# Kernel tuning notes

Hardware: AMD Instinct MI355X
Metric: run time of the kernel (lower is better)

The kernel has to match this reference:

```python
import jax, jax.numpy as jnp
import numpy as np
from jax import lax

B, H, W = 4096, 8, 8
DICT, SE, E, NZ = 64, 8, 256, 1024
C1, C2 = 64, 128
EPS = 1e-4


def setup_inputs() -> dict:
    key = jax.random.key(0)
    ks = jax.random.split(key, 32)
    d = {}
    d['s'] = jax.random.randint(ks[0], (B, H, W), 0, DICT)
    d['s_prime'] = jax.random.randint(ks[1], (B, H, W), 0, DICT)
    d['w_embed'] = jax.random.normal(ks[2], (DICT, SE), dtype=jnp.float32)
    i = 3
    for p in ('p1', 'p2', 'p3'):
        d[p + '_w1'] = jax.random.normal(ks[i], (C1, SE, 3, 3), dtype=jnp.float32) * 0.1; i += 1
        d[p + '_b1'] = jax.random.normal(ks[i], (C1,), dtype=jnp.float32) * 0.1; i += 1
        d[p + '_w2'] = jax.random.normal(ks[i], (C2, C1, 3, 3), dtype=jnp.float32) * 0.05; i += 1
        d[p + '_b2'] = jax.random.normal(ks[i], (C2,), dtype=jnp.float32) * 0.05; i += 1
        d[p + '_lw'] = jax.random.normal(ks[i], (E, C2 * H * W), dtype=jnp.float32) * 0.02; i += 1
        d[p + '_lb'] = jax.random.normal(ks[i], (E,), dtype=jnp.float32) * 0.02; i += 1
    d['z_vectors'] = jax.random.normal(ks[i], (NZ, E), dtype=jnp.float32)
    d['scale'] = jnp.ones((1,), dtype=jnp.float32)
    return d


def _conv(x, w, b):
    # x: [B,C,H,W], w: [O,I,3,3], padding=1 == SAME for k=3
    y = lax.conv_general_dilated(x, w, (1, 1), 'SAME',
                                 dimension_numbers=('NCHW', 'OIHW', 'NCHW'))
    return y + b[None, :, None, None]


def _phi(x, w1, b1, w2, b2, lw, lb):
    # run_modules(..., last_activation=True): relu after every conv
    x = jax.nn.relu(_conv(x, w1, b1))
    x = jax.nn.relu(_conv(x, w2, b2))
    x = x.reshape(x.shape[0], -1)  # [B, C2*H*W]
    return x @ lw.T + lb  # [B, E]


def _normalized(m, eps):
    return m / (jnp.sqrt(jnp.sum(m * m, axis=1, keepdims=True)) + eps)


def reference(s, s_prime, w_embed,
              p1_w1, p1_b1, p1_w2, p1_b2, p1_lw, p1_lb,
              p2_w1, p2_b1, p2_w2, p2_b2, p2_lw, p2_lb,
              p3_w1, p3_b1, p3_w2, p3_b2, p3_lw, p3_lb,
              z_vectors, scale):
    # nn.Embedding(max_norm=1): renorm rows with norm > 1 to unit norm
    wn = jnp.sqrt(jnp.sum(w_embed * w_embed, axis=1, keepdims=True))
    w = w_embed * jnp.minimum(1.0, 1.0 / jnp.maximum(wn, 1e-7))
    s_embed = jnp.transpose(w[s], (0, 3, 1, 2))        # [B,SE,H,W]
    sp_embed = jnp.transpose(w[s_prime], (0, 3, 1, 2))  # embed_conv is None -> identity

    s_int = _phi(s_embed, p1_w1, p1_b1, p1_w2, p1_b2, p1_lw, p1_lb)            # phi1
    diff_int = _phi(sp_embed - s_embed, p2_w1, p2_b1, p2_w2, p2_b2, p2_lw, p2_lb)  # phi2
    sp_out = _normalized(_phi(sp_embed, p3_w1, p3_b1, p3_w2, p3_b2, p3_lw, p3_lb), EPS)  # phi3

    # quantize: cdist (p=2) against codebook, argmax (farthest, as in source), gather
    x2 = jnp.sum(diff_int * diff_int, axis=1, keepdims=True)      # [B,1]
    z2 = jnp.sum(z_vectors * z_vectors, axis=1)[None, :]          # [1,NZ]
    dist = jnp.sqrt(jnp.maximum(x2 + z2 - 2.0 * (diff_int @ z_vectors.T), 0.0))  # [B,NZ]
    z_inds = jnp.argmax(dist, axis=1)                              # [B]
    z_matrix = z_vectors[z_inds]                                   # [B,E]

    s_out = _normalized(s_int + z_matrix, EPS)                     # fc (fc_sizes=None)
    gram = s_out @ sp_out.T                                        # [B,B]
    return jnp.exp(scale) * gram
```

## Files before the change

kernel.cpp:

```cpp
#include <hip/hip_runtime.h>
#include <hip/hip_bf16.h>
#include <math.h>

#define NB 4096
#define SE 8
#define ND 64
#define C1 64
#define C2 128
#define NE 256
#define NZ 1024
#define CHUNK 2048
#define KACT 8192
#define KSPLIT 8

#define W1M_N (3*12*64*8)
#define W2M_N (3*18*128*32)
#define ZT_N  (256*1024)
#define PREP_TOTAL (W1M_N + W2M_N + ZT_N)
#define PREP_TOTAL2 (PREP_TOTAL + 512)
#define LW_N (NE*KACT)

typedef __attribute__((ext_vector_type(8))) short bf16x8;
typedef __attribute__((ext_vector_type(4))) float f32x4;
typedef __attribute__((ext_vector_type(8))) unsigned short u16x8;
typedef __attribute__((ext_vector_type(4))) unsigned short u16x4;

static __device__ __forceinline__ unsigned short f2bf(float v) {
  __hip_bfloat16 h = __float2bfloat16(v);
  return __builtin_bit_cast(unsigned short, h);
}
static __device__ __forceinline__ float bf2f(unsigned short u) {
  return __bfloat162float(__builtin_bit_cast(__hip_bfloat16, u));
}

__global__ __launch_bounds__(256) void prep_kernel(
    const float* __restrict__ w1_0, const float* __restrict__ w1_1, const float* __restrict__ w1_2,
    const float* __restrict__ w2_0, const float* __restrict__ w2_1, const float* __restrict__ w2_2,
    const float* __restrict__ z, const float* __restrict__ w_embed,
    unsigned short* __restrict__ w1mh, unsigned short* __restrict__ w1ml,
    unsigned short* __restrict__ w2mh, unsigned short* __restrict__ w2ml,
    float* __restrict__ zT, float* __restrict__ wnorm)
{
  int idx = blockIdx.x * 256 + threadIdx.x;
  if (idx < W1M_N) {
    int p = idx / 6144; int r = idx - p*6144;
    int j = r >> 9; int rem = r & 511; int o = rem >> 3; int c = rem & 7;
    const float* w1 = (p == 0) ? w1_0 : (p == 1) ? w1_1 : w1_2;
    float v = (j < 9) ? w1[o*72 + c*9 + j] : 0.f;
    unsigned short h = f2bf(v);
    w1mh[idx] = h;
    w1ml[idx] = f2bf(v - bf2f(h));
  } else if (idx < W1M_N + W2M_N) {
    int r0 = idx - W1M_N;
    int p = r0 / (128*576); int r = r0 - p*(128*576);
    int o = r / 576; int rem = r - o*576; int j = rem >> 6; int c = rem & 63;
    const float* w2 = (p == 0) ? w2_0 : (p == 1) ? w2_1 : w2_2;
    float v = w2[o*576 + c*9 + j];
    unsigned short h = f2bf(v);
    const int d = p*(128*576) + ((j << 1) + (c >> 5))*4096 + o*32 + (c & 31);
    w2mh[d] = h;
    w2ml[d] = f2bf(v - bf2f(h));
  } else if (idx < PREP_TOTAL) {
    int r = idx - (W1M_N + W2M_N);
    int e = r >> 10, n = r & 1023;
    zT[r] = z[n*256 + e];
  } else if (idx < PREP_TOTAL2) {
    int t = idx - PREP_TOTAL;
    int o = t >> 3, c = t & 7;
    float ss = 0.f;
    #pragma unroll
    for (int e = 0; e < 8; ++e) { float u = w_embed[o*8 + e]; ss += u*u; }
    float nrm = sqrtf(ss);
    float sc = fminf(1.f, 1.f / fmaxf(nrm, 1e-7f));
    wnorm[o*8 + c] = w_embed[o*8 + c] * sc;
  }
}

__global__ __launch_bounds__(256) void prep_lw_kernel(
    const float* __restrict__ lw, unsigned short* __restrict__ lwh,
    unsigned short* __restrict__ lwl, int do_lo)
{
  int idx = blockIdx.x * 256 + threadIdx.x;
  float v = lw[idx];
  unsigned short h = f2bf(v);
  lwh[idx] = h;
  if (do_lo) lwl[idx] = f2bf(v - bf2f(h));
}

template<int PASSES>
__global__ __launch_bounds__(256, 4) void conv_phi_kernel(
    const int* __restrict__ s, const int* __restrict__ sp,
    const float* __restrict__ wnorm,
    const unsigned short* __restrict__ w1mh, const unsigned short* __restrict__ w1ml,
    const float* __restrict__ b1,
    const unsigned short* __restrict__ w2mh, const unsigned short* __restrict__ w2ml,
    const float* __restrict__ b2,
    unsigned short* __restrict__ acth, unsigned short* __restrict__ actl,
    int mode, int b_start)
{
  __shared__ __align__(16) unsigned short xph[960];
  __shared__ __align__(16) unsigned short xpl[960];
  __shared__ __align__(16) unsigned short c1h[7680];
  __shared__ __align__(16) unsigned short c1l[7680];

  const int tid = threadIdx.x;
  const int b = b_start + blockIdx.x;

  {
    int4 z4 = {0,0,0,0};
    for (int t = tid; t < 120; t += 256) { ((int4*)xph)[t] = z4; ((int4*)xpl)[t] = z4; }
    for (int t = tid; t < 960; t += 256) { ((int4*)c1h)[t] = z4; ((int4*)c1l)[t] = z4; }
  }
  __syncthreads();

  if (tid < 64) {
    const int si  = s[b*64 + tid];
    const int spi = sp[b*64 + tid];
    const float4 a0 = *(const float4*)(wnorm + si*8);
    const float4 a1v = *(const float4*)(wnorm + si*8 + 4);
    const float4 c0 = *(const float4*)(wnorm + spi*8);
    const float4 c1v = *(const float4*)(wnorm + spi*8 + 4);
    float e0[8] = {a0.x,a0.y,a0.z,a0.w, a1v.x,a1v.y,a1v.z,a1v.w};
    float e1[8] = {c0.x,c0.y,c0.z,c0.w, c1v.x,c1v.y,c1v.z,c1v.w};
    u16x8 hv, lv;
    #pragma unroll
    for (int c = 0; c < SE; ++c) {
      float v = (mode == 0) ? e0[c] : (mode == 1) ? (e1[c] - e0[c]) : e1[c];
      unsigned short h = f2bf(v);
      hv[c] = h;
      lv[c] = f2bf(v - bf2f(h));
    }
    const int lin = ((tid >> 3) + 1)*12 + (tid & 7) + 1;
    *(u16x8*)(xph + lin*8) = hv;
    *(u16x8*)(xpl + lin*8) = lv;
  }
  __syncthreads();

  {
    const int lane = tid & 63, wid = tid >> 6;
    const int ph = wid;
    const int l15 = lane & 15, lk4 = lane >> 4;

    f32x4 a1[4];
    #pragma unroll
    for (int fm = 0; fm < 4; ++fm) a1[fm] = (f32x4){0.f,0.f,0.f,0.f};

    #pragma unroll
    for (int kk = 0; kk < 3; ++kk) {
      const int j = (kk << 2) + lk4;
      const int jc = (j > 8) ? 8 : j;
      const int dy = jc / 3, dx = jc - 3*(jc/3);
      bf16x8 Wh[4], Wl[4];
      #pragma unroll
      for (int fm = 0; fm < 4; ++fm) {
        const int o = (fm << 4) + l15;
        Wh[fm] = *(const bf16x8*)(w1mh + (j << 9) + (o << 3));
        Wl[fm] = *(const bf16x8*)(w1ml + (j << 9) + (o << 3));
      }
      const int p = (ph << 4) + l15;
      const int lin = ((p >> 3) + dy)*12 + (p & 7) + dx;
      const bf16x8 Xh = *(const bf16x8*)(xph + (lin << 3));
      const bf16x8 Xl = *(const bf16x8*)(xpl + (lin << 3));
      __builtin_amdgcn_s_setprio(1);
      #pragma unroll
      for (int fm = 0; fm < 4; ++fm) {
        a1[fm] = __builtin_amdgcn_mfma_f32_16x16x32_bf16(Wh[fm], Xh, a1[fm], 0, 0, 0);
        a1[fm] = __builtin_amdgcn_mfma_f32_16x16x32_bf16(Wl[fm], Xh, a1[fm], 0, 0, 0);
        a1[fm] = __builtin_amdgcn_mfma_f32_16x16x32_bf16(Wh[fm], Xl, a1[fm], 0, 0, 0);
      }
      __builtin_amdgcn_s_setprio(0);
    }

    const int p = (ph << 4) + l15;
    const int lin = ((p >> 3) + 1)*12 + (p & 7) + 1;
    #pragma unroll
    for (int fm = 0; fm < 4; ++fm) {
      const int obase = (fm << 4) + (lk4 << 2);
      const float4 bv = *(const float4*)(b1 + obase);
      const int idx2 = (obase >> 3)*960 + lin*8 + (obase & 7);
      u16x4 hv, lv;
      {
        float v0 = fmaxf(a1[fm][0] + bv.x, 0.f);
        float v1 = fmaxf(a1[fm][1] + bv.y, 0.f);
        float v2 = fmaxf(a1[fm][2] + bv.z, 0.f);
        float v3 = fmaxf(a1[fm][3] + bv.w, 0.f);
        hv[0] = f2bf(v0); hv[1] = f2bf(v1); hv[2] = f2bf(v2); hv[3] = f2bf(v3);
        lv[0] = f2bf(v0 - bf2f(hv[0])); lv[1] = f2bf(v1 - bf2f(hv[1]));
        lv[2] = f2bf(v2 - bf2f(hv[2])); lv[3] = f2bf(v3 - bf2f(hv[3]));
      }
      *(u16x4*)(c1h + idx2) = hv;
      *(u16x4*)(c1l + idx2) = lv;
    }
  }
  __syncthreads();

  {
    const int lane = tid & 63, wid = tid >> 6;
    const int ob = wid << 5;
    const int l15 = lane & 15, lk4 = lane >> 4;
    const int y0b = l15 >> 3, x0 = l15 & 7;

    f32x4 acc[4][2];
    #pragma unroll
    for (int mf = 0; mf < 4; ++mf)
      #pragma unroll
      for (int nf = 0; nf < 2; ++nf) acc[mf][nf] = (f32x4){0.f,0.f,0.f,0.f};

    #pragma unroll
    for (int j = 0; j < 9; ++j) {
      const int dy = j / 3, dx = j - 3*(j/3);
      #pragma unroll
      for (int h2 = 0; h2 < 2; ++h2) {
        const int sbase = ((j << 1) + h2) << 12;
        bf16x8 Bh[2], Bl[2];
        #pragma unroll
        for (int nf = 0; nf < 2; ++nf) {
          const int orow = ob + (nf << 4) + l15;
          const int a = sbase + orow*32 + (lk4 << 3);
          Bh[nf] = *(const bf16x8*)(w2mh + a);
          if (PASSES == 3) Bl[nf] = *(const bf16x8*)(w2ml + a);
        }
        const int cbk = (h2 << 2) + lk4;
        bf16x8 Ah[4], Al[4];
        #pragma unroll
        for (int mf = 0; mf < 4; ++mf) {
          const int lin = ((mf << 1) + y0b + dy)*12 + x0 + dx;
          const int a = cbk*960 + (lin << 3);
          Ah[mf] = *(const bf16x8*)(c1h + a);
          Al[mf] = *(const bf16x8*)(c1l + a);
        }
        __builtin_amdgcn_s_setprio(1);
        #pragma unroll
        for (int mf = 0; mf < 4; ++mf) {
          #pragma unroll
          for (int nf = 0; nf < 2; ++nf) {
            acc[mf][nf] = __builtin_amdgcn_mfma_f32_16x16x32_bf16(Ah[mf], Bh[nf], acc[mf][nf], 0, 0, 0);
            acc[mf][nf] = __builtin_amdgcn_mfma_f32_16x16x32_bf16(Al[mf], Bh[nf], acc[mf][nf], 0, 0, 0);
            if (PASSES == 3)
              acc[mf][nf] = __builtin_amdgcn_mfma_f32_16x16x32_bf16(Ah[mf], Bl[nf], acc[mf][nf], 0, 0, 0);
          }
        }
        __builtin_amdgcn_s_setprio(0);
      }
    }

    const size_t rowbase = (size_t)blockIdx.x * 8192;
    #pragma unroll
    for (int nf = 0; nf < 2; ++nf) {
      const int col = ob + (nf << 4) + l15;
      const float bv = b2[col];
      #pragma unroll
      for (int mf = 0; mf < 4; ++mf) {
        const int p0 = mf*16 + lk4*4;
        u16x4 hv, lv;
        #pragma unroll
        for (int r2 = 0; r2 < 4; ++r2) {
          float v = fmaxf(acc[mf][nf][r2] + bv, 0.f);
          unsigned short hq = f2bf(v);
          hv[r2] = hq;
          lv[r2] = f2bf(v - bf2f(hq));
        }
        *(u16x4*)(acth + rowbase + col*64 + p0) = hv;
        if (PASSES == 3)
          *(u16x4*)(actl + rowbase + col*64 + p0) = lv;
      }
    }
  }
}

template<int PASSES>
__global__ __launch_bounds__(256) void gemm_lds_tn(
    const unsigned short* __restrict__ Ahp, const unsigned short* __restrict__ Alp,
    const unsigned short* __restrict__ Bhp, const unsigned short* __restrict__ Blp,
    int K, float* __restrict__ Cdirect, float* __restrict__ Cpart,
    const float* __restrict__ bias, const float* __restrict__ scale_ptr)
{
  constexpr int NOP = (PASSES == 3) ? 2 : 1;
  __shared__ __align__(16) unsigned short As[NOP][128*64];
  __shared__ __align__(16) unsigned short Bs[NOP][64*64];

  const int tid = threadIdx.x;
  const int lane = tid & 63, wid = tid >> 6;
  const int wm = wid >> 1, wn = wid & 1;
  const int l15 = lane & 15, lk4 = lane >> 4;
  const int M = gridDim.x << 7, N = gridDim.y << 6;
  const int KC = K / gridDim.z;
  const int bm = blockIdx.x << 7, bn = blockIdx.y << 6;
  const int kbase = blockIdx.z * KC;
  const int NT = KC >> 6;

  const int sr = tid >> 3;
  const int sc8 = (tid & 7) * 8;

  const unsigned short* gA[NOP];
  const unsigned short* gB[NOP];
  gA[0] = Ahp; gB[0] = Bhp;
  if (PASSES == 3) { gA[1] = Alp; gB[1] = Blp; }

  u16x8 ra[NOP][4], rb[NOP][2];

  f32x4 acc[4][2];
  #pragma unroll
  for (int fm = 0; fm < 4; ++fm)
    #pragma unroll
    for (int nf = 0; nf < 2; ++nf) acc[fm][nf] = (f32x4){0.f,0.f,0.f,0.f};

  {
    const int k0 = kbase + sc8;
    #pragma unroll
    for (int p = 0; p < NOP; ++p) {
      #pragma unroll
      for (int i = 0; i < 4; ++i)
        ra[p][i] = *(const u16x8*)(gA[p] + (size_t)(bm + sr + i*32) * K + k0);
      #pragma unroll
      for (int i = 0; i < 2; ++i)
        rb[p][i] = *(const u16x8*)(gB[p] + (size_t)(bn + sr + i*32) * K + k0);
    }
  }

  for (int t = 0; t < NT; ++t) {
    __syncthreads();
    #pragma unroll
    for (int p = 0; p < NOP; ++p) {
      #pragma unroll
      for (int i = 0; i < 4; ++i) {
        const int r = sr + i*32;
        *(u16x8*)(&As[p][r*64 + (sc8 ^ ((r & 7) << 3))]) = ra[p][i];
      }
      #pragma unroll
      for (int i = 0; i < 2; ++i) {
        const int r = sr + i*32;
        *(u16x8*)(&Bs[p][r*64 + (sc8 ^ ((r & 7) << 3))]) = rb[p][i];
      }
    }
    __syncthreads();
    if (t + 1 < NT) {
      const int k0 = kbase + ((t + 1) << 6) + sc8;
      #pragma unroll
      for (int p = 0; p < NOP; ++p) {
        #pragma unroll
        for (int i = 0; i < 4; ++i)
          ra[p][i] = *(const u16x8*)(gA[p] + (size_t)(bm + sr + i*32) * K + k0);
        #pragma unroll
        for (int i = 0; i < 2; ++i)
          rb[p][i] = *(const u16x8*)(gB[p] + (size_t)(bn + sr + i*32) * K + k0);
      }
    }
    #pragma unroll
    for (int ks = 0; ks < 2; ++ks) {
      const int kb = ks*32 + lk4*8;
      bf16x8 af[NOP][4], bf[NOP][2];
      #pragma unroll
      for (int p = 0; p < NOP; ++p) {
        #pragma unroll
        for (int fm = 0; fm < 4; ++fm) {
          const int r = wm*64 + fm*16 + l15;
          af[p][fm] = *(const bf16x8*)(&As[p][r*64 + (kb ^ ((r & 7) << 3))]);
        }
        #pragma unroll
        for (int nf = 0; nf < 2; ++nf) {
          const int r = wn*32 + nf*16 + l15;
          bf[p][nf] = *(const bf16x8*)(&Bs[p][r*64 + (kb ^ ((r & 7) << 3))]);
        }
      }
      #pragma unroll
      for (int fm = 0; fm < 4; ++fm) {
        #pragma unroll
        for (int nf = 0; nf < 2; ++nf) {
          acc[fm][nf] = __builtin_amdgcn_mfma_f32_16x16x32_bf16(af[0][fm], bf[0][nf], acc[fm][nf], 0, 0, 0);
          if (PASSES == 3) {
            acc[fm][nf] = __builtin_amdgcn_mfma_f32_16x16x32_bf16(af[0][fm], bf[1][nf], acc[fm][nf], 0, 0, 0);
            acc[fm][nf] = __builtin_amdgcn_mfma_f32_16x16x32_bf16(af[1][fm], bf[0][nf], acc[fm][nf], 0, 0, 0);
          }
        }
      }
    }
  }

  if (Cpart) {
    float* base = Cpart + (size_t)blockIdx.z * ((size_t)M * N);
    #pragma unroll
    for (int fm = 0; fm < 4; ++fm) {
      #pragma unroll
      for (int nf = 0; nf < 2; ++nf) {
        const int row0 = bm + wm*64 + fm*16 + lk4*4;
        const int col  = bn + wn*32 + nf*16 + l15;
        #pragma unroll
        for (int r2 = 0; r2 < 4; ++r2)
          base[(size_t)(row0 + r2) * N + col] = acc[fm][nf][r2];
      }
    }
  } else {
    float alpha = scale_ptr ? expf(scale_ptr[0]) : 1.f;
    #pragma unroll
    for (int fm = 0; fm < 4; ++fm) {
      #pragma unroll
      for (int nf = 0; nf < 2; ++nf) {
        const int row0 = bm + wm*64 + fm*16 + lk4*4;
        const int col  = bn + wn*32 + nf*16 + l15;
        const float bv = bias ? bias[col] : 0.f;
        #pragma unroll
        for (int r2 = 0; r2 < 4; ++r2)
          Cdirect[(size_t)(row0 + r2) * N + col] = alpha * acc[fm][nf][r2] + bv;
      }
    }
  }
}

__global__ __launch_bounds__(256) void reduce_bias_kernel(
    const float* __restrict__ part, const float* __restrict__ bias, float* __restrict__ out)
{
  const int idx = blockIdx.x * 256 + threadIdx.x;
  float a = bias[idx & (NE-1)];
  #pragma unroll
  for (int q = 0; q < KSPLIT; ++q) a += part[(size_t)q * (CHUNK*NE) + idx];
  out[idx] = a;
}

__global__ __launch_bounds__(256) void quant_kernel(
    const float* __restrict__ diff, const float* __restrict__ zT, int* __restrict__ z_ind)
{
  __shared__ __align__(16) float d[8][NE];
  __shared__ float wv[8][4];
  __shared__ int wni[8][4];
  const int tid = threadIdx.x;
  const int b0 = blockIdx.x * 8;
  for (int j = tid; j < 8*NE; j += 256) (&d[0][0])[j] = diff[(size_t)b0*NE + j];
  __syncthreads();

  float zz[4] = {0.f, 0.f, 0.f, 0.f};
  float dot[8][4] = {};
  for (int e = 0; e < NE; e += 4) {
    float4 dd[8];
    #pragma unroll
    for (int r = 0; r < 8; ++r) dd[r] = *(const float4*)(&d[r][e]);
    #pragma unroll
    for (int u = 0; u < 4; ++u) {
      const float* zr = zT + (size_t)(e + u) * NZ + tid;
      float z0 = zr[0], z1 = zr[256], z2 = zr[512], z3 = zr[768];
      zz[0] = fmaf(z0, z0, zz[0]); zz[1] = fmaf(z1, z1, zz[1]);
      zz[2] = fmaf(z2, z2, zz[2]); zz[3] = fmaf(z3, z3, zz[3]);
      #pragma unroll
      for (int r = 0; r < 8; ++r) {
        const float de = (u == 0) ? dd[r].x : (u == 1) ? dd[r].y : (u == 2) ? dd[r].z : dd[r].w;
        dot[r][0] = fmaf(z0, de, dot[r][0]);
        dot[r][1] = fmaf(z1, de, dot[r][1]);
        dot[r][2] = fmaf(z2, de, dot[r][2]);
        dot[r][3] = fmaf(z3, de, dot[r][3]);
      }
    }
  }

  const int lane = tid & 63, wid = tid >> 6;
  #pragma unroll
  for (int r = 0; r < 8; ++r) {
    float best = zz[0] - 2.f*dot[r][0]; int bi = tid;
    float v1 = zz[1] - 2.f*dot[r][1]; if (v1 > best) { best = v1; bi = tid + 256; }
    float v2 = zz[2] - 2.f*dot[r][2]; if (v2 > best) { best = v2; bi = tid + 512; }
    float v3 = zz[3] - 2.f*dot[r][3]; if (v3 > best) { best = v3; bi = tid + 768; }
    for (int m = 1; m < 64; m <<= 1) {
      float ov = __shfl_xor(best, m, 64);
      int   oi = __shfl_xor(bi, m, 64);
      if (ov > best || (ov == best && oi < bi)) { best = ov; bi = oi; }
    }
    if (lane == 0) { wv[r][wid] = best; wni[r][wid] = bi; }
  }
  __syncthreads();
  if (tid < 8) {
    float best = wv[tid][0]; int bi = wni[tid][0];
    #pragma unroll
    for (int w = 1; w < 4; ++w) {
      float v = wv[tid][w]; int n = wni[tid][w];
      if (v > best || (v == best && n < bi)) { best = v; bi = n; }
    }
    z_ind[b0 + tid] = bi;
  }
}

__global__ __launch_bounds__(256) void norm_to_bf16_kernel(
    const float* __restrict__ v, unsigned short* __restrict__ ob)
{
  const int row = blockIdx.x*4 + (threadIdx.x >> 6);
  const int lane = threadIdx.x & 63;
  float4 x = ((const float4*)v)[(size_t)row*64 + lane];
  float ss = x.x*x.x + x.y*x.y + x.z*x.z + x.w*x.w;
  #pragma unroll
  for (int m = 1; m < 64; m <<= 1) ss += __shfl_xor(ss, m, 64);
  float sc = 1.f / (sqrtf(ss) + 1e-4f);
  u16x4 o;
  o[0] = f2bf(x.x*sc); o[1] = f2bf(x.y*sc); o[2] = f2bf(x.z*sc); o[3] = f2bf(x.w*sc);
  *(u16x4*)(ob + (size_t)row*NE + lane*4) = o;
}

__global__ __launch_bounds__(256) void build_sout_kernel(
    const float* __restrict__ s_int, const float* __restrict__ z,
    const int* __restrict__ z_ind, unsigned short* __restrict__ ob)
{
  const int row = blockIdx.x*4 + (threadIdx.x >> 6);
  const int lane = threadIdx.x & 63;
  const int zi = z_ind[row];
  float4 a = *((const float4*)s_int + (size_t)row*64 + lane);
  float4 c = *((const float4*)z + (size_t)zi*64 + lane);
  float4 x = {a.x + c.x, a.y + c.y, a.z + c.z, a.w + c.w};
  float ss = x.x*x.x + x.y*x.y + x.z*x.z + x.w*x.w;
  #pragma unroll
  for (int m = 1; m < 64; m <<= 1) ss += __shfl_xor(ss, m, 64);
  float sc = 1.f / (sqrtf(ss) + 1e-4f);
  u16x4 o;
  o[0] = f2bf(x.x*sc); o[1] = f2bf(x.y*sc); o[2] = f2bf(x.z*sc); o[3] = f2bf(x.w*sc);
  *(u16x4*)(ob + (size_t)row*NE + lane*4) = o;
}

extern "C" void kernel_launch(void* const* d_in, const int* in_sizes, int n_in,
                              void* d_out, int out_size, void* d_ws, size_t ws_size,
                              hipStream_t stream)
{
  const int* s  = (const int*)d_in[0];
  const int* sp = (const int*)d_in[1];
  const float* w_embed = (const float*)d_in[2];
  const float* z = (const float*)d_in[21];
  const float* scale = (const float*)d_in[22];
  float* out = (float*)d_out;

  size_t off = 0;
  auto allocB = [&](size_t bytes) -> void* {
    void* p = (void*)((char*)d_ws + off);
    off += ((bytes + 255) & ~(size_t)255);
    return p;
  };
  unsigned short* w1mh  = (unsigned short*)allocB((size_t)W1M_N * 2);
  unsigned short* w1ml  = (unsigned short*)allocB((size_t)W1M_N * 2);
  unsigned short* w2mh  = (unsigned short*)allocB((size_t)W2M_N * 2);
  unsigned short* w2ml  = (unsigned short*)allocB((size_t)W2M_N * 2);
  float* zT             = (float*)allocB(ZT_N * 4);
  float* wnorm          = (float*)allocB(64 * 8 * 4);
  unsigned short* lwh   = (unsigned short*)allocB((size_t)LW_N * 2);
  unsigned short* lwl   = (unsigned short*)allocB((size_t)LW_N * 2);
  float* s_int          = (float*)allocB((size_t)NB * NE * 4);
  float* diff_int       = (float*)allocB((size_t)NB * NE * 4);
  float* sp_out         = (float*)allocB((size_t)NB * NE * 4);
  unsigned short* soutb = (unsigned short*)allocB((size_t)NB * NE * 2);
  unsigned short* spoutb= (unsigned short*)allocB((size_t)NB * NE * 2);
  int*   z_ind          = (int*)allocB(NB * 4);
  float* part           = (float*)allocB((size_t)CHUNK * NE * KSPLIT * 4);

  unsigned short* acth = (unsigned short*)d_out;
  unsigned short* actl = acth + (size_t)CHUNK * KACT;

  prep_kernel<<<PREP_TOTAL2/256, 256, 0, stream>>>(
      (const float*)d_in[3],  (const float*)d_in[9],  (const float*)d_in[15],
      (const float*)d_in[5],  (const float*)d_in[11], (const float*)d_in[17],
      z, w_embed, w1mh, w1ml, w2mh, w2ml, zT, wnorm);

  for (int phi = 0; phi < 3; ++phi) {
    const float* b1 = (const float*)d_in[4 + phi*6];
    const float* b2 = (const float*)d_in[6 + phi*6];
    const float* lw = (const float*)d_in[7 + phi*6];
    const float* lb = (const float*)d_in[8 + phi*6];
    float* outvec = (phi == 0) ? s_int : (phi == 1) ? diff_int : sp_out;

    prep_lw_kernel<<<LW_N/256, 256, 0, stream>>>(lw, lwh, lwl, phi == 1);

    for (int b0 = 0; b0 < NB; b0 += CHUNK) {
      if (phi == 1)
        conv_phi_kernel<3><<<CHUNK, 256, 0, stream>>>(
            s, sp, wnorm, w1mh + phi*6144, w1ml + phi*6144, b1,
            w2mh + phi*(128*576), w2ml + phi*(128*576), b2,
            acth, actl, phi, b0);
      else
        conv_phi_kernel<2><<<CHUNK, 256, 0, stream>>>(
            s, sp, wnorm, w1mh + phi*6144, w1ml + phi*6144, b1,
            w2mh + phi*(128*576), w2ml + phi*(128*576), b2,
            acth, actl, phi, b0);
      dim3 g(CHUNK/128, NE/64, KSPLIT);
      if (phi == 1)
        gemm_lds_tn<3><<<g, 256, 0, stream>>>(acth, actl, lwh, lwl,
            KACT, nullptr, part, nullptr, nullptr);
      else
        gemm_lds_tn<1><<<g, 256, 0, stream>>>(acth, nullptr, lwh, nullptr,
            KACT, nullptr, part, nullptr, nullptr);
      reduce_bias_kernel<<<(CHUNK*NE)/256, 256, 0, stream>>>(part, lb, outvec + (size_t)b0*NE);
    }
  }

  norm_to_bf16_kernel<<<NB/4, 256, 0, stream>>>(sp_out, spoutb);
  quant_kernel<<<NB/8, 256, 0, stream>>>(diff_int, zT, z_ind);
  build_sout_kernel<<<NB/4, 256, 0, stream>>>(s_int, z, z_ind, soutb);

  dim3 gg(NB/128, NB/64, 1);
  gemm_lds_tn<1><<<gg, 256, 0, stream>>>(soutb, nullptr, spoutb, nullptr,
      NE, out, nullptr, nullptr, scale);
}
```

Before: 527.0 us.

## Replace split-K partial buffer and reduce kernel with atomic accumulation; pad conv LDS

The split-K linear GEMM now adds its partial results straight into the output vector with atomicAdd. The output is pre-filled with the bias inside prep_lw_kernel, so the partial-sum buffer and the separate reduce_bias kernel launches are no longer needed. Separately, the per-channel-group stride of the conv1 activation buffer in LDS is padded from 960 to 968 elements, meant to cut bank conflicts on the conv2 operand loads. The cost is atomic contention from 8 K-splits and a summation order that is no longer deterministic.

```diff
diff --git a/kernel.cpp b/kernel.cpp
--- a/kernel.cpp
+++ b/kernel.cpp
@@ -12,6 +12,7 @@
 #define CHUNK 2048
 #define KACT 8192
 #define KSPLIT 8
+#define C1PAD 968
 
 #define W1M_N (3*12*64*8)
 #define W2M_N (3*18*128*32)
@@ -78,13 +79,15 @@
 
 __global__ __launch_bounds__(256) void prep_lw_kernel(
     const float* __restrict__ lw, unsigned short* __restrict__ lwh,
-    unsigned short* __restrict__ lwl, int do_lo)
+    unsigned short* __restrict__ lwl, int do_lo,
+    float* __restrict__ outvec, const float* __restrict__ lb)
 {
   int idx = blockIdx.x * 256 + threadIdx.x;
   float v = lw[idx];
   unsigned short h = f2bf(v);
   lwh[idx] = h;
   if (do_lo) lwl[idx] = f2bf(v - bf2f(h));
+  if (idx < NB*NE) outvec[idx] = lb[idx & (NE-1)];
 }
 
 template<int PASSES>
@@ -100,8 +103,8 @@
 {
   __shared__ __align__(16) unsigned short xph[960];
   __shared__ __align__(16) unsigned short xpl[960];
-  __shared__ __align__(16) unsigned short c1h[7680];
-  __shared__ __align__(16) unsigned short c1l[7680];
+  __shared__ __align__(16) unsigned short c1h[8*C1PAD];
+  __shared__ __align__(16) unsigned short c1l[8*C1PAD];
 
   const int tid = threadIdx.x;
   const int b = b_start + blockIdx.x;
@@ -109,7 +112,7 @@
   {
     int4 z4 = {0,0,0,0};
     for (int t = tid; t < 120; t += 256) { ((int4*)xph)[t] = z4; ((int4*)xpl)[t] = z4; }
-    for (int t = tid; t < 960; t += 256) { ((int4*)c1h)[t] = z4; ((int4*)c1l)[t] = z4; }
+    for (int t = tid; t < C1PAD; t += 256) { ((int4*)c1h)[t] = z4; ((int4*)c1l)[t] = z4; }
   }
   __syncthreads();
 
@@ -177,7 +180,7 @@
     for (int fm = 0; fm < 4; ++fm) {
       const int obase = (fm << 4) + (lk4 << 2);
       const float4 bv = *(const float4*)(b1 + obase);
-      const int idx2 = (obase >> 3)*960 + lin*8 + (obase & 7);
+      const int idx2 = (obase >> 3)*C1PAD + lin*8 + (obase & 7);
       u16x4 hv, lv;
       {
         float v0 = fmaxf(a1[fm][0] + bv.x, 0.f);
@@ -225,7 +228,7 @@
         #pragma unroll
         for (int mf = 0; mf < 4; ++mf) {
           const int lin = ((mf << 1) + y0b + dy)*12 + x0 + dx;
-          const int a = cbk*960 + (lin << 3);
+          const int a = cbk*C1PAD + (lin << 3);
           Ah[mf] = *(const bf16x8*)(c1h + a);
           Al[mf] = *(const bf16x8*)(c1l + a);
         }
@@ -378,7 +381,6 @@
   }
 
   if (Cpart) {
-    float* base = Cpart + (size_t)blockIdx.z * ((size_t)M * N);
     #pragma unroll
     for (int fm = 0; fm < 4; ++fm) {
       #pragma unroll
@@ -387,7 +389,7 @@
         const int col  = bn + wn*32 + nf*16 + l15;
         #pragma unroll
         for (int r2 = 0; r2 < 4; ++r2)
-          base[(size_t)(row0 + r2) * N + col] = acc[fm][nf][r2];
+          atomicAdd(Cpart + (size_t)(row0 + r2) * N + col, acc[fm][nf][r2]);
       }
     }
   } else {
@@ -405,16 +407,6 @@
       }
     }
   }
-}
-
-__global__ __launch_bounds__(256) void reduce_bias_kernel(
-    const float* __restrict__ part, const float* __restrict__ bias, float* __restrict__ out)
-{
-  const int idx = blockIdx.x * 256 + threadIdx.x;
-  float a = bias[idx & (NE-1)];
-  #pragma unroll
-  for (int q = 0; q < KSPLIT; ++q) a += part[(size_t)q * (CHUNK*NE) + idx];
-  out[idx] = a;
 }
 
 __global__ __launch_bounds__(256) void quant_kernel(
@@ -542,7 +534,6 @@
   unsigned short* soutb = (unsigned short*)allocB((size_t)NB * NE * 2);
   unsigned short* spoutb= (unsigned short*)allocB((size_t)NB * NE * 2);
   int*   z_ind          = (int*)allocB(NB * 4);
-  float* part           = (float*)allocB((size_t)CHUNK * NE * KSPLIT * 4);
 
   unsigned short* acth = (unsigned short*)d_out;
   unsigned short* actl = acth + (size_t)CHUNK * KACT;
@@ -559,7 +550,7 @@
     const float* lb = (const float*)d_in[8 + phi*6];
     float* outvec = (phi == 0) ? s_int : (phi == 1) ? diff_int : sp_out;
 
-    prep_lw_kernel<<<LW_N/256, 256, 0, stream>>>(lw, lwh, lwl, phi == 1);
+    prep_lw_kernel<<<LW_N/256, 256, 0, stream>>>(lw, lwh, lwl, phi == 1, outvec, lb);
 
     for (int b0 = 0; b0 < NB; b0 += CHUNK) {
       if (phi == 1)
@@ -575,11 +566,10 @@
       dim3 g(CHUNK/128, NE/64, KSPLIT);
       if (phi == 1)
         gemm_lds_tn<3><<<g, 256, 0, stream>>>(acth, actl, lwh, lwl,
-            KACT, nullptr, part, nullptr, nullptr);
+            KACT, nullptr, outvec + (size_t)b0*NE, nullptr, nullptr);
       else
         gemm_lds_tn<1><<<g, 256, 0, stream>>>(acth, nullptr, lwh, nullptr,
-            KACT, nullptr, part, nullptr, nullptr);
-      reduce_bias_kernel<<<(CHUNK*NE)/256, 256, 0, stream>>>(part, lb, outvec + (size_t)b0*NE);
+            KACT, nullptr, outvec + (size_t)b0*NE, nullptr, nullptr);
     }
   }
 
```

Measured after the change: 564.5 us. 7.1% more time.
